# Performance work log

Measured on AMD Instinct MI355X. Metric: run time of the kernel, lower is better.

The kernel has to match this reference:

```python
import jax, jax.numpy as jnp
import numpy as np

D_MODEL = 512
N_HEADS = 8
D_K = D_MODEL // N_HEADS


def setup_inputs() -> dict:
    key = jax.random.key(0)
    ks = jax.random.split(key, 9)
    s = 1.0 / np.sqrt(D_MODEL)
    x = jax.random.normal(ks[0], (2, 4096, D_MODEL), dtype=jnp.float32)
    def lin(kw, kb):
        W = jax.random.uniform(kw, (D_MODEL, D_MODEL), jnp.float32, -s, s)
        b = jax.random.uniform(kb, (D_MODEL,), jnp.float32, -s, s)
        return W, b
    Wq, bq = lin(ks[1], ks[2])
    Wk, bk = lin(ks[3], ks[4])
    Wv, bv = lin(ks[5], ks[6])
    Wo, bo = lin(ks[7], ks[8])
    return {"x": x, "Wq": Wq, "bq": bq, "Wk": Wk, "bk": bk,
            "Wv": Wv, "bv": bv, "Wo": Wo, "bo": bo}


def reference(x, Wq, bq, Wk, bk, Wv, bv, Wo, bo):
    B, T, C = x.shape
    # project and split heads: [B, H, T, d_k]
    def heads(W, b):
        return (x @ W.T + b).reshape(B, T, N_HEADS, D_K).transpose(0, 2, 1, 3)
    q = heads(Wq, bq)
    k = heads(Wk, bk)
    v = heads(Wv, bv)
    scores = jnp.einsum('bhqd,bhkd->bhqk', q, k) / np.sqrt(D_K).astype(jnp.float32)
    attn = jax.nn.softmax(scores, axis=-1)  # dropout p=0 (eval)
    out = jnp.einsum('bhqk,bhkd->bhqd', attn, v)
    out = out.transpose(0, 2, 1, 3).reshape(B, T, C)
    return out @ Wo.T + bo
```

## Files before the change

### kernel.cpp

```cpp
#include <hip/hip_runtime.h>

typedef _Float16 f16x8 __attribute__((ext_vector_type(8)));
typedef _Float16 f16x4 __attribute__((ext_vector_type(4)));
typedef _Float16 f16x2 __attribute__((ext_vector_type(2)));
typedef __fp16 hf16x2 __attribute__((ext_vector_type(2)));
typedef float f32x4 __attribute__((ext_vector_type(4)));

__device__ __forceinline__ float fast_exp2(float x) {
#if __has_builtin(__builtin_amdgcn_exp2f)
  return __builtin_amdgcn_exp2f(x);
#else
  return exp2f(x);
#endif
}

__device__ __forceinline__ f16x2 pk_cvt(float a, float b) {
#if __has_builtin(__builtin_amdgcn_cvt_pkrtz)
  union { hf16x2 h; f16x2 f; } u;
  u.h = __builtin_amdgcn_cvt_pkrtz(a, b);
  return u.f;
#else
  f16x2 r; r[0] = (_Float16)a; r[1] = (_Float16)b; return r;
#endif
}

__device__ __forceinline__ void qswap32(int& x, int& y) {
  asm("v_permlane32_swap_b32 %0, %1" : "+v"(x), "+v"(y));
}

__device__ __forceinline__ int swz23(int c) {
  return (c & ~12) | ((c & 4) << 1) | ((c & 8) >> 1);
}

__global__ void cvt_all(const float* __restrict__ x,
                        const float* __restrict__ Wq, const float* __restrict__ Wk,
                        const float* __restrict__ Wv, const float* __restrict__ Wo,
                        _Float16* __restrict__ xf, _Float16* __restrict__ wf) {
  int g = blockIdx.x * blockDim.x + threadIdx.x;
  const float* src;
  _Float16* dst;
  if (g < 524288) {
    src = x + (size_t)g * 8;
    dst = xf + (size_t)g * 8;
  } else {
    int g2 = g - 524288;
    int z = g2 >> 15, off = g2 & 32767;
    const float* W = (z == 0) ? Wq : (z == 1) ? Wk : (z == 2) ? Wv : Wo;
    src = W + (size_t)off * 8;
    dst = wf + (size_t)z * 262144 + (size_t)off * 8;
  }
  f32x4 a = *(const f32x4*)src;
  f32x4 b = *(const f32x4*)(src + 4);
  f16x8 o;
  o[0] = (_Float16)a[0]; o[1] = (_Float16)a[1];
  o[2] = (_Float16)a[2]; o[3] = (_Float16)a[3];
  o[4] = (_Float16)b[0]; o[5] = (_Float16)b[1];
  o[6] = (_Float16)b[2]; o[7] = (_Float16)b[3];
  *(f16x8*)dst = o;
}

__global__ __launch_bounds__(256, 2)
void qkv_gemm(const _Float16* __restrict__ X, const _Float16* __restrict__ Wf,
              const float* __restrict__ bq, const float* __restrict__ bk,
              const float* __restrict__ bv, _Float16* __restrict__ dst3) {
  __shared__ __align__(16) _Float16 As[128][72];
  __shared__ __align__(16) _Float16 Bs[128][72];
  const int z = blockIdx.z;
  const _Float16* Wz = Wf + (size_t)z * 262144;
  const float* bias = (z == 0) ? bq : (z == 1 ? bk : bv);
  _Float16* dst = dst3 + (size_t)z * 4194304;
  const float scale = (z == 0) ? 0.18033688011112042f : 1.0f;

  const int t = threadIdx.x;
  const int lane = t & 63, wave = t >> 6;
  const int quad = lane >> 4, col = lane & 15;
  const int wm = (wave & 1) * 64, wn = (wave >> 1) * 64;
  const int m0 = blockIdx.x * 128, n0 = blockIdx.y * 128;

  f32x4 acc[4][4] = {};

  if (z != 2) {
    for (int k0 = 0; k0 < 512; k0 += 64) {
      __syncthreads();
#pragma unroll
      for (int i = 0; i < 4; i++) {
        int flat = i * 2048 + t * 8;
        int r = flat >> 6, c = flat & 63;
        *(f16x8*)&As[r][c] = *(const f16x8*)&X[(size_t)(m0 + r) * 512 + k0 + c];
        *(f16x8*)&Bs[r][c] = *(const f16x8*)&Wz[(size_t)(n0 + r) * 512 + k0 + c];
      }
      __syncthreads();
#pragma unroll
      for (int ks = 0; ks < 2; ks++) {
        f16x8 a[4], b[4];
#pragma unroll
        for (int i = 0; i < 4; i++) {
          a[i] = *(const f16x8*)&As[wm + i * 16 + col][ks * 32 + quad * 8];
          b[i] = *(const f16x8*)&Bs[wn + i * 16 + col][ks * 32 + quad * 8];
        }
#pragma unroll
        for (int mi = 0; mi < 4; mi++)
#pragma unroll
          for (int ni = 0; ni < 4; ni++)
            acc[mi][ni] = __builtin_amdgcn_mfma_f32_16x16x32_f16(b[ni], a[mi], acc[mi][ni], 0, 0, 0);
      }
    }
#pragma unroll
    for (int ni = 0; ni < 4; ni++) {
      int nb = n0 + wn + ni * 16 + quad * 4;
      int h = nb >> 6, d0 = nb & 63;
      f32x4 bb = *(const f32x4*)&bias[nb];
#pragma unroll
      for (int mi = 0; mi < 4; mi++) {
        int m = m0 + wm + mi * 16 + col;
        int b = m >> 12, tt = m & 4095;
        f16x4 ov;
#pragma unroll
        for (int r = 0; r < 4; r++)
          ov[r] = (_Float16)((acc[mi][ni][r] + bb[r]) * scale);
        *(f16x4*)&dst[((size_t)(b * 8 + h) * 4096 + tt) * 64 + d0] = ov;
      }
    }
  } else {
    for (int k0 = 0; k0 < 512; k0 += 64) {
      __syncthreads();
#pragma unroll
      for (int i = 0; i < 4; i++) {
        int flat = i * 2048 + t * 8;
        int r = flat >> 6, c = flat & 63;
        *(f16x8*)&As[r][c] = *(const f16x8*)&X[(size_t)(m0 + r) * 512 + k0 + c];
        *(f16x8*)&Bs[r][c] = *(const f16x8*)&Wz[(size_t)(n0 + r) * 512 + k0 + c];
      }
      __syncthreads();
#pragma unroll
      for (int ks = 0; ks < 2; ks++) {
        f16x8 a[4], b[4];
#pragma unroll
        for (int i = 0; i < 4; i++) {
          a[i] = *(const f16x8*)&As[wm + i * 16 + col][ks * 32 + quad * 8];
          b[i] = *(const f16x8*)&Bs[wn + i * 16 + col][ks * 32 + quad * 8];
        }
#pragma unroll
        for (int mi = 0; mi < 4; mi++)
#pragma unroll
          for (int ni = 0; ni < 4; ni++)
            acc[mi][ni] = __builtin_amdgcn_mfma_f32_16x16x32_f16(a[mi], b[ni], acc[mi][ni], 0, 0, 0);
      }
    }
#pragma unroll
    for (int ni = 0; ni < 4; ni++) {
      int n = n0 + wn + ni * 16 + col;
      float bv_ = bias[n];
      int h = n >> 6, d = n & 63;
#pragma unroll
      for (int mi = 0; mi < 4; mi++) {
        int m = m0 + wm + mi * 16 + quad * 4;
        int b = m >> 12, tt = m & 4095;
        f16x4 ov;
#pragma unroll
        for (int r = 0; r < 4; r++) ov[r] = (_Float16)(acc[mi][ni][r] + bv_);
        *(f16x4*)&dst[((size_t)((b * 8 + h) * 64 + d)) * 4096 + tt] = ov;
      }
    }
  }
}

__global__ __launch_bounds__(256, 4)
void attn_kernel(const _Float16* __restrict__ Q, const _Float16* __restrict__ K,
                 const _Float16* __restrict__ V, _Float16* __restrict__ O) {
  __shared__ __align__(16) _Float16 Ks[2][64][72];
  __shared__ __align__(16) _Float16 Vt[2][64][72];

  const int t = threadIdx.x;
  const int lane = t & 63, wave = t >> 6;
  const int quad = lane >> 4, col = lane & 15;
  const int id = blockIdx.y * 32 + blockIdx.x;
  const int xcd = id & 7, slot = id >> 3;
  const int bh = xcd * 2 + (slot >> 5);
  const int q0 = (slot & 31) * 128;
  const _Float16* Qb = Q + (size_t)bh * 4096 * 64;
  const _Float16* Kbh = K + (size_t)bh * 4096 * 64;
  const _Float16* Vg = V + (size_t)bh * 64 * 4096;

  const int sr = (t * 8) >> 6, sc = (t * 8) & 63;
  const int vrow = t >> 3, vcol = (t & 7) * 8;
  const int vc0 = swz23(vcol);
  const int vc1 = swz23(vcol + 4);

  f16x8 qf[2][2];
#pragma unroll
  for (int mt = 0; mt < 2; mt++)
#pragma unroll
    for (int ks = 0; ks < 2; ks++)
      qf[mt][ks] = *(const f16x8*)&Qb[(size_t)(q0 + wave * 32 + mt * 16 + col) * 64 +
                                      ks * 32 + quad * 8];

  const f32x4 fz = {0.f, 0.f, 0.f, 0.f};

  f16x8 kreg[2], vreg[2];
#pragma unroll
  for (int i = 0; i < 2; i++)
    kreg[i] = *(const f16x8*)&Kbh[(size_t)(sr + 32 * i) * 64 + sc];
#pragma unroll
  for (int it = 0; it < 2; it++)
    vreg[it] = *(const f16x8*)&Vg[(size_t)(it * 32 + vrow) * 4096 + vcol];
#pragma unroll
  for (int i = 0; i < 2; i++)
    *(f16x8*)&Ks[0][sr + 32 * i][sc] = kreg[i];
#pragma unroll
  for (int it = 0; it < 2; it++) {
    f16x4 lo, hi;
#pragma unroll
    for (int u = 0; u < 4; u++) { lo[u] = vreg[it][u]; hi[u] = vreg[it][u + 4]; }
    *(f16x4*)&Vt[0][it * 32 + vrow][vc0] = lo;
    *(f16x4*)&Vt[0][it * 32 + vrow][vc1] = hi;
  }
  __syncthreads();

  f32x4 o_acc[2][4] = {};
  float lsum[2] = {0.f, 0.f};

  for (int j = 0; j < 64; j++) {
    const int buf = j & 1;
    if (j + 1 < 64) {
      const _Float16* Kb = Kbh + (size_t)(j + 1) * 64 * 64;
#pragma unroll
      for (int i = 0; i < 2; i++)
        kreg[i] = *(const f16x8*)&Kb[(size_t)(sr + 32 * i) * 64 + sc];
#pragma unroll
      for (int it = 0; it < 2; it++)
        vreg[it] = *(const f16x8*)&Vg[(size_t)(it * 32 + vrow) * 4096 +
                                      (j + 1) * 64 + vcol];
    }

    f32x4 s[2][4];
    __builtin_amdgcn_s_setprio(1);
#pragma unroll
    for (int nt = 0; nt < 4; nt++) {
      f16x8 kf = *(const f16x8*)&Ks[buf][nt * 16 + col][quad * 8];
#pragma unroll
      for (int mt = 0; mt < 2; mt++)
        s[mt][nt] = __builtin_amdgcn_mfma_f32_16x16x32_f16(kf, qf[mt][0], fz, 0, 0, 0);
    }
#pragma unroll
    for (int nt = 0; nt < 4; nt++) {
      f16x8 kf = *(const f16x8*)&Ks[buf][nt * 16 + col][32 + quad * 8];
#pragma unroll
      for (int mt = 0; mt < 2; mt++)
        s[mt][nt] = __builtin_amdgcn_mfma_f32_16x16x32_f16(kf, qf[mt][1], s[mt][nt], 0, 0, 0);
    }
    __builtin_amdgcn_s_setprio(0);

    f16x4 pf[2][4];
#pragma unroll
    for (int mt = 0; mt < 2; mt++) {
#pragma unroll
      for (int nt = 0; nt < 4; nt++) {
        float p0 = fast_exp2(s[mt][nt][0]);
        float p1 = fast_exp2(s[mt][nt][1]);
        float p2 = fast_exp2(s[mt][nt][2]);
        float p3 = fast_exp2(s[mt][nt][3]);
        lsum[mt] += (p0 + p1) + (p2 + p3);
        union { f16x4 v4; f16x2 v2[2]; } u;
        u.v2[0] = pk_cvt(p0, p1);
        u.v2[1] = pk_cvt(p2, p3);
        pf[mt][nt] = u.v4;
      }
    }

    __builtin_amdgcn_s_setprio(1);
#pragma unroll
    for (int u = 0; u < 2; u++) {
      f16x8 p8[2];
#pragma unroll
      for (int mt = 0; mt < 2; mt++) {
        union { f16x4 v; int d[2]; } X, Y;
        X.v = pf[mt][2 * u]; Y.v = pf[mt][2 * u + 1];
        int x0 = X.d[0], y0 = Y.d[0], x1 = X.d[1], y1 = Y.d[1];
        qswap32(x0, y0);
        qswap32(x1, y1);
        union { int d[4]; f16x8 v; } P;
        P.d[0] = x0; P.d[1] = x1; P.d[2] = y0; P.d[3] = y1;
        p8[mt] = P.v;
      }
#pragma unroll
      for (int dt = 0; dt < 4; dt++) {
        f16x8 vf = *(const f16x8*)&Vt[buf][dt * 16 + col][u * 32 + quad * 8];
#pragma unroll
        for (int mt = 0; mt < 2; mt++)
          o_acc[mt][dt] = __builtin_amdgcn_mfma_f32_16x16x32_f16(vf, p8[mt], o_acc[mt][dt], 0, 0, 0);
      }
    }
    __builtin_amdgcn_s_setprio(0);

    if (j + 1 < 64) {
      const int nb = buf ^ 1;
#pragma unroll
      for (int i = 0; i < 2; i++)
        *(f16x8*)&Ks[nb][sr + 32 * i][sc] = kreg[i];
#pragma unroll
      for (int it = 0; it < 2; it++) {
        f16x4 lo, hi;
#pragma unroll
        for (int u = 0; u < 4; u++) { lo[u] = vreg[it][u]; hi[u] = vreg[it][u + 4]; }
        *(f16x4*)&Vt[nb][it * 32 + vrow][vc0] = lo;
        *(f16x4*)&Vt[nb][it * 32 + vrow][vc1] = hi;
      }
      __syncthreads();
    }
  }

  const int b = bh >> 3, h = bh & 7;
#pragma unroll
  for (int mt = 0; mt < 2; mt++) {
    float l = lsum[mt];
    l += __shfl_xor(l, 16, 64);
    l += __shfl_xor(l, 32, 64);
    int row = q0 + wave * 32 + mt * 16 + col;
    float inv = 1.0f / l;
#pragma unroll
    for (int dt = 0; dt < 4; dt++) {
      f16x4 ov;
#pragma unroll
      for (int r = 0; r < 4; r++) ov[r] = (_Float16)(o_acc[mt][dt][r] * inv);
      *(f16x4*)&O[((size_t)(b * 4096 + row)) * 512 + h * 64 + dt * 16 + quad * 4] = ov;
    }
  }
}

__global__ __launch_bounds__(256, 2)
void out_gemm(const _Float16* __restrict__ X, const _Float16* __restrict__ Wo,
              const float* __restrict__ bias, float* __restrict__ out) {
  __shared__ __align__(16) _Float16 As[128][72];
  __shared__ __align__(16) _Float16 Bs[128][72];
  const int t = threadIdx.x;
  const int lane = t & 63, wave = t >> 6;
  const int quad = lane >> 4, col = lane & 15;
  const int wm = (wave & 1) * 64, wn = (wave >> 1) * 64;
  const int m0 = blockIdx.x * 128, n0 = blockIdx.y * 128;

  f32x4 acc[4][4] = {};

  for (int k0 = 0; k0 < 512; k0 += 64) {
    __syncthreads();
#pragma unroll
    for (int i = 0; i < 4; i++) {
      int flat = i * 2048 + t * 8;
      int r = flat >> 6, c = flat & 63;
      *(f16x8*)&As[r][c] = *(const f16x8*)&X[(size_t)(m0 + r) * 512 + k0 + c];
      *(f16x8*)&Bs[r][c] = *(const f16x8*)&Wo[(size_t)(n0 + r) * 512 + k0 + c];
    }
    __syncthreads();
#pragma unroll
    for (int ks = 0; ks < 2; ks++) {
      f16x8 a[4], b[4];
#pragma unroll
      for (int i = 0; i < 4; i++) {
        a[i] = *(const f16x8*)&As[wm + i * 16 + col][ks * 32 + quad * 8];
        b[i] = *(const f16x8*)&Bs[wn + i * 16 + col][ks * 32 + quad * 8];
      }
#pragma unroll
      for (int mi = 0; mi < 4; mi++)
#pragma unroll
        for (int ni = 0; ni < 4; ni++)
          acc[mi][ni] = __builtin_amdgcn_mfma_f32_16x16x32_f16(a[mi], b[ni], acc[mi][ni], 0, 0, 0);
    }
  }

#pragma unroll
  for (int ni = 0; ni < 4; ni++) {
    int n = n0 + wn + ni * 16 + col;
    float bv_ = bias[n];
#pragma unroll
    for (int mi = 0; mi < 4; mi++) {
#pragma unroll
      for (int r = 0; r < 4; r++) {
        int m = m0 + wm + mi * 16 + quad * 4 + r;
        out[(size_t)m * 512 + n] = acc[mi][ni][r] + bv_;
      }
    }
  }
}

extern "C" void kernel_launch(void* const* d_in, const int* in_sizes, int n_in,
                              void* d_out, int out_size, void* d_ws, size_t ws_size,
                              hipStream_t stream) {
  const float* x  = (const float*)d_in[0];
  const float* Wq = (const float*)d_in[1];
  const float* bq = (const float*)d_in[2];
  const float* Wk = (const float*)d_in[3];
  const float* bk = (const float*)d_in[4];
  const float* Wv = (const float*)d_in[5];
  const float* bv = (const float*)d_in[6];
  const float* Wo = (const float*)d_in[7];
  const float* bo = (const float*)d_in[8];

  char* ws = (char*)d_ws;
  _Float16* xf  = (_Float16*)(ws);
  _Float16* wf  = (_Float16*)(ws + (8u << 20));
  _Float16* qkv = (_Float16*)(ws + (10u << 20));
  _Float16* ao  = (_Float16*)(ws);

  cvt_all<<<2560, 256, 0, stream>>>(x, Wq, Wk, Wv, Wo, xf, wf);

  qkv_gemm<<<dim3(64, 4, 3), 256, 0, stream>>>(xf, wf, bq, bk, bv, qkv);

  attn_kernel<<<dim3(32, 16), 256, 0, stream>>>(qkv, qkv + 4194304,
                                                qkv + 2 * 4194304, ao);

  out_gemm<<<dim3(64, 4), 256, 0, stream>>>(ao, wf + 3 * 262144, bo,
                                            (float*)d_out);
}
```

Baseline: 199.5 us.

## Software-pipeline attention loop: overlap next-tile QK^T with current PV using triple-buffered LDS

Restructures the attention main loop so the QK^T MFMAs for tile j+1 are issued before the exp/PV work of tile j, using two alternating score register sets and a triple-buffered K/V LDS ring. One barrier per iteration now separates staging from compute, and the global loads for tile j+2 are issued in between. This aims to hide exp latency and global-load latency behind MFMA work. It costs more registers and LDS, so launch bounds drop from 4 to 2 blocks per CU, which may reduce occupancy.

```diff
diff --git a/kernel.cpp b/kernel.cpp
--- a/kernel.cpp
+++ b/kernel.cpp
@@ -165,11 +165,11 @@
   }
 }
 
-__global__ __launch_bounds__(256, 4)
+__global__ __launch_bounds__(256, 2)
 void attn_kernel(const _Float16* __restrict__ Q, const _Float16* __restrict__ K,
                  const _Float16* __restrict__ V, _Float16* __restrict__ O) {
-  __shared__ __align__(16) _Float16 Ks[2][64][72];
-  __shared__ __align__(16) _Float16 Vt[2][64][72];
+  __shared__ __align__(16) _Float16 Ks[3][64][72];
+  __shared__ __align__(16) _Float16 Vt[3][64][72];
 
   const int t = threadIdx.x;
   const int lane = t & 63, wave = t >> 6;
@@ -198,117 +198,123 @@
   const f32x4 fz = {0.f, 0.f, 0.f, 0.f};
 
   f16x8 kreg[2], vreg[2];
-#pragma unroll
-  for (int i = 0; i < 2; i++)
-    kreg[i] = *(const f16x8*)&Kbh[(size_t)(sr + 32 * i) * 64 + sc];
-#pragma unroll
-  for (int it = 0; it < 2; it++)
-    vreg[it] = *(const f16x8*)&Vg[(size_t)(it * 32 + vrow) * 4096 + vcol];
-#pragma unroll
-  for (int i = 0; i < 2; i++)
-    *(f16x8*)&Ks[0][sr + 32 * i][sc] = kreg[i];
-#pragma unroll
-  for (int it = 0; it < 2; it++) {
-    f16x4 lo, hi;
-#pragma unroll
-    for (int u = 0; u < 4; u++) { lo[u] = vreg[it][u]; hi[u] = vreg[it][u + 4]; }
-    *(f16x4*)&Vt[0][it * 32 + vrow][vc0] = lo;
-    *(f16x4*)&Vt[0][it * 32 + vrow][vc1] = hi;
-  }
-  __syncthreads();
-
+  f32x4 sA[2][4], sB[2][4];
   f32x4 o_acc[2][4] = {};
   float lsum[2] = {0.f, 0.f};
 
-  for (int j = 0; j < 64; j++) {
-    const int buf = j & 1;
-    if (j + 1 < 64) {
-      const _Float16* Kb = Kbh + (size_t)(j + 1) * 64 * 64;
-#pragma unroll
-      for (int i = 0; i < 2; i++)
-        kreg[i] = *(const f16x8*)&Kb[(size_t)(sr + 32 * i) * 64 + sc];
-#pragma unroll
-      for (int it = 0; it < 2; it++)
-        vreg[it] = *(const f16x8*)&Vg[(size_t)(it * 32 + vrow) * 4096 +
-                                      (j + 1) * 64 + vcol];
-    }
-
-    f32x4 s[2][4];
-    __builtin_amdgcn_s_setprio(1);
-#pragma unroll
-    for (int nt = 0; nt < 4; nt++) {
-      f16x8 kf = *(const f16x8*)&Ks[buf][nt * 16 + col][quad * 8];
-#pragma unroll
-      for (int mt = 0; mt < 2; mt++)
-        s[mt][nt] = __builtin_amdgcn_mfma_f32_16x16x32_f16(kf, qf[mt][0], fz, 0, 0, 0);
-    }
-#pragma unroll
-    for (int nt = 0; nt < 4; nt++) {
-      f16x8 kf = *(const f16x8*)&Ks[buf][nt * 16 + col][32 + quad * 8];
-#pragma unroll
-      for (int mt = 0; mt < 2; mt++)
-        s[mt][nt] = __builtin_amdgcn_mfma_f32_16x16x32_f16(kf, qf[mt][1], s[mt][nt], 0, 0, 0);
-    }
-    __builtin_amdgcn_s_setprio(0);
-
-    f16x4 pf[2][4];
-#pragma unroll
-    for (int mt = 0; mt < 2; mt++) {
-#pragma unroll
-      for (int nt = 0; nt < 4; nt++) {
-        float p0 = fast_exp2(s[mt][nt][0]);
-        float p1 = fast_exp2(s[mt][nt][1]);
-        float p2 = fast_exp2(s[mt][nt][2]);
-        float p3 = fast_exp2(s[mt][nt][3]);
-        lsum[mt] += (p0 + p1) + (p2 + p3);
-        union { f16x4 v4; f16x2 v2[2]; } u;
-        u.v2[0] = pk_cvt(p0, p1);
-        u.v2[1] = pk_cvt(p2, p3);
-        pf[mt][nt] = u.v4;
-      }
-    }
-
-    __builtin_amdgcn_s_setprio(1);
-#pragma unroll
-    for (int u = 0; u < 2; u++) {
-      f16x8 p8[2];
-#pragma unroll
-      for (int mt = 0; mt < 2; mt++) {
-        union { f16x4 v; int d[2]; } X, Y;
-        X.v = pf[mt][2 * u]; Y.v = pf[mt][2 * u + 1];
-        int x0 = X.d[0], y0 = Y.d[0], x1 = X.d[1], y1 = Y.d[1];
-        qswap32(x0, y0);
-        qswap32(x1, y1);
-        union { int d[4]; f16x8 v; } P;
-        P.d[0] = x0; P.d[1] = x1; P.d[2] = y0; P.d[3] = y1;
-        p8[mt] = P.v;
-      }
-#pragma unroll
-      for (int dt = 0; dt < 4; dt++) {
-        f16x8 vf = *(const f16x8*)&Vt[buf][dt * 16 + col][u * 32 + quad * 8];
-#pragma unroll
-        for (int mt = 0; mt < 2; mt++)
-          o_acc[mt][dt] = __builtin_amdgcn_mfma_f32_16x16x32_f16(vf, p8[mt], o_acc[mt][dt], 0, 0, 0);
-      }
-    }
-    __builtin_amdgcn_s_setprio(0);
-
-    if (j + 1 < 64) {
-      const int nb = buf ^ 1;
-#pragma unroll
-      for (int i = 0; i < 2; i++)
-        *(f16x8*)&Ks[nb][sr + 32 * i][sc] = kreg[i];
-#pragma unroll
-      for (int it = 0; it < 2; it++) {
-        f16x4 lo, hi;
-#pragma unroll
-        for (int u = 0; u < 4; u++) { lo[u] = vreg[it][u]; hi[u] = vreg[it][u + 4]; }
-        *(f16x4*)&Vt[nb][it * 32 + vrow][vc0] = lo;
-        *(f16x4*)&Vt[nb][it * 32 + vrow][vc1] = hi;
-      }
-      __syncthreads();
-    }
-  }
+#define LOADT(J)                                                              \
+  {                                                                           \
+    const _Float16* Kb_ = Kbh + (size_t)(J) * 64 * 64;                        \
+    _Pragma("unroll") for (int i = 0; i < 2; i++)                             \
+      kreg[i] = *(const f16x8*)&Kb_[(size_t)(sr + 32 * i) * 64 + sc];         \
+    _Pragma("unroll") for (int it = 0; it < 2; it++)                          \
+      vreg[it] = *(const f16x8*)&Vg[(size_t)(it * 32 + vrow) * 4096 +         \
+                                    (size_t)(J) * 64 + vcol];                 \
+  }
+
+#define STAGE(NB)                                                             \
+  {                                                                           \
+    _Pragma("unroll") for (int i = 0; i < 2; i++)                             \
+      *(f16x8*)&Ks[(NB)][sr + 32 * i][sc] = kreg[i];                          \
+    _Pragma("unroll") for (int it = 0; it < 2; it++) {                        \
+      f16x4 lo, hi;                                                           \
+      _Pragma("unroll") for (int u = 0; u < 4; u++) {                         \
+        lo[u] = vreg[it][u]; hi[u] = vreg[it][u + 4];                         \
+      }                                                                       \
+      *(f16x4*)&Vt[(NB)][it * 32 + vrow][vc0] = lo;                           \
+      *(f16x4*)&Vt[(NB)][it * 32 + vrow][vc1] = hi;                           \
+    }                                                                         \
+  }
+
+#define QKT(NB, S)                                                            \
+  {                                                                           \
+    __builtin_amdgcn_s_setprio(1);                                            \
+    _Pragma("unroll") for (int nt = 0; nt < 4; nt++) {                        \
+      f16x8 kf = *(const f16x8*)&Ks[(NB)][nt * 16 + col][quad * 8];           \
+      _Pragma("unroll") for (int mt = 0; mt < 2; mt++)                        \
+        S[mt][nt] = __builtin_amdgcn_mfma_f32_16x16x32_f16(kf, qf[mt][0],     \
+                                                           fz, 0, 0, 0);      \
+    }                                                                         \
+    _Pragma("unroll") for (int nt = 0; nt < 4; nt++) {                        \
+      f16x8 kf = *(const f16x8*)&Ks[(NB)][nt * 16 + col][32 + quad * 8];      \
+      _Pragma("unroll") for (int mt = 0; mt < 2; mt++)                        \
+        S[mt][nt] = __builtin_amdgcn_mfma_f32_16x16x32_f16(kf, qf[mt][1],     \
+                                                           S[mt][nt], 0, 0, 0); \
+    }                                                                         \
+    __builtin_amdgcn_s_setprio(0);                                            \
+  }
+
+#define EXPPV(CB, S)                                                          \
+  {                                                                           \
+    f16x4 pf[2][4];                                                           \
+    _Pragma("unroll") for (int mt = 0; mt < 2; mt++)                          \
+      _Pragma("unroll") for (int nt = 0; nt < 4; nt++) {                      \
+        float p0 = fast_exp2(S[mt][nt][0]);                                   \
+        float p1 = fast_exp2(S[mt][nt][1]);                                   \
+        float p2 = fast_exp2(S[mt][nt][2]);                                   \
+        float p3 = fast_exp2(S[mt][nt][3]);                                   \
+        lsum[mt] += (p0 + p1) + (p2 + p3);                                    \
+        union { f16x4 v4; f16x2 v2[2]; } u_;                                  \
+        u_.v2[0] = pk_cvt(p0, p1);                                            \
+        u_.v2[1] = pk_cvt(p2, p3);                                            \
+        pf[mt][nt] = u_.v4;                                                   \
+      }                                                                       \
+    __builtin_amdgcn_s_setprio(1);                                            \
+    _Pragma("unroll") for (int u = 0; u < 2; u++) {                           \
+      f16x8 p8[2];                                                            \
+      _Pragma("unroll") for (int mt = 0; mt < 2; mt++) {                      \
+        union { f16x4 v; int d[2]; } X_, Y_;                                  \
+        X_.v = pf[mt][2 * u]; Y_.v = pf[mt][2 * u + 1];                       \
+        int x0 = X_.d[0], y0 = Y_.d[0], x1 = X_.d[1], y1 = Y_.d[1];           \
+        qswap32(x0, y0);                                                      \
+        qswap32(x1, y1);                                                      \
+        union { int d[4]; f16x8 v; } P_;                                      \
+        P_.d[0] = x0; P_.d[1] = x1; P_.d[2] = y0; P_.d[3] = y1;               \
+        p8[mt] = P_.v;                                                        \
+      }                                                                       \
+      _Pragma("unroll") for (int dt = 0; dt < 4; dt++) {                      \
+        f16x8 vf = *(const f16x8*)&Vt[(CB)][dt * 16 + col][u * 32 + quad * 8]; \
+        _Pragma("unroll") for (int mt = 0; mt < 2; mt++)                      \
+          o_acc[mt][dt] = __builtin_amdgcn_mfma_f32_16x16x32_f16(             \
+              vf, p8[mt], o_acc[mt][dt], 0, 0, 0);                            \
+      }                                                                       \
+    }                                                                         \
+    __builtin_amdgcn_s_setprio(0);                                            \
+  }
+
+#define PBODY(CUR, NXT, CONS, PROD, JLOAD, DOLOAD)                            \
+  {                                                                           \
+    STAGE(NXT);                                                               \
+    __syncthreads();                                                          \
+    QKT(NXT, PROD);                                                           \
+    if (DOLOAD) LOADT(JLOAD);                                                 \
+    EXPPV(CUR, CONS);                                                         \
+  }
+
+  LOADT(0);
+  STAGE(0);
+  LOADT(1);
+  __syncthreads();
+  QKT(0, sA);
+
+  for (int jt = 0; jt < 60; jt += 6) {
+    PBODY(0, 1, sA, sB, jt + 2, true);
+    PBODY(1, 2, sB, sA, jt + 3, true);
+    PBODY(2, 0, sA, sB, jt + 4, true);
+    PBODY(0, 1, sB, sA, jt + 5, true);
+    PBODY(1, 2, sA, sB, jt + 6, true);
+    PBODY(2, 0, sB, sA, jt + 7, true);
+  }
+  PBODY(0, 1, sA, sB, 62, true);
+  PBODY(1, 2, sB, sA, 63, true);
+  PBODY(2, 0, sA, sB, 0, false);
+  EXPPV(0, sB);
+
+#undef LOADT
+#undef STAGE
+#undef QKT
+#undef EXPPV
+#undef PBODY
 
   const int b = bh >> 3, h = bh & 7;
 #pragma unroll
```

Result: no change. 196.4 us (-1.6%).
